# Optimization experiments

Hardware: AMD Instinct MI355X
Metric: run time of the kernel (lower is better)

Reference implementation:

```python
import jax, jax.numpy as jnp
import numpy as np
import math

D_MODEL = 1024
NUM_HEADS = 16
D_K = D_MODEL // NUM_HEADS
ROPE_THETA = 10000.0


def _rope(x, pos):
    # x: [b, h, s, d], pos: [s] int -> apply interleaved rotary embedding
    d = x.shape[-1]
    inv_freq = 1.0 / (ROPE_THETA ** (jnp.arange(0, d, 2, dtype=jnp.float32) / d))  # [d/2]
    angles = pos.astype(jnp.float32)[:, None] * inv_freq  # [s, d/2]
    cos = jnp.cos(angles)  # broadcast to [1,1,s,d/2]
    sin = jnp.sin(angles)
    x1 = x[..., 0::2]
    x2 = x[..., 1::2]
    o1 = x1 * cos - x2 * sin
    o2 = x1 * sin + x2 * cos
    return jnp.stack([o1, o2], axis=-1).reshape(x.shape)


def setup_inputs() -> dict:
    key = jax.random.key(0)
    kx, kq, kk, kv, ko = jax.random.split(key, 5)
    scale = 1.0 / math.sqrt(D_MODEL)
    x = jax.random.normal(kx, (2, 2048, D_MODEL), dtype=jnp.float32)
    token_positions = jnp.arange(2048, dtype=jnp.int32)
    Wq = jax.random.normal(kq, (D_MODEL, D_MODEL), dtype=jnp.float32) * scale
    Wk = jax.random.normal(kk, (D_MODEL, D_MODEL), dtype=jnp.float32) * scale
    Wv = jax.random.normal(kv, (D_MODEL, D_MODEL), dtype=jnp.float32) * scale
    Wo = jax.random.normal(ko, (D_MODEL, D_MODEL), dtype=jnp.float32) * scale
    return {"x": x, "token_positions": token_positions, "Wq": Wq, "Wk": Wk, "Wv": Wv, "Wo": Wo}


def reference(x, token_positions, Wq, Wk, Wv, Wo):
    b, s, _ = x.shape
    h, dk = NUM_HEADS, D_K
    # Linear stores weight as [out, in]; y = x @ W.T
    def proj(W):
        y = jnp.einsum('bsm,nm->bsn', x, W)
        return y.reshape(b, s, h, dk).transpose(0, 2, 1, 3)  # [b,h,s,dk]
    Q = _rope(proj(Wq), token_positions)
    K = _rope(proj(Wk), token_positions)
    V = proj(Wv)
    scores = jnp.einsum('bhqd,bhkd->bhqk', Q, K) / math.sqrt(dk)
    causal = jnp.arange(s)[:, None] >= jnp.arange(s)[None, :]  # [s,s]
    scores = jnp.where(causal, scores, -jnp.inf)
    weights = jax.nn.softmax(scores, axis=-1)
    attn = jnp.einsum('bhqk,bhkd->bhqd', weights, V)  # [b,h,s,dk]
    attn = attn.transpose(0, 2, 1, 3).reshape(b, s, h * dk)
    return jnp.einsum('bsn,mn->bsm', attn, Wo)
```

## Files before the change

kernel.cpp:

```cpp
#include <hip/hip_runtime.h>
#include <math.h>

#define SEQ   2048
#define BATCH 2
#define NH    16
#define DKD   64
#define DM    1024
#define MTOT  (BATCH*SEQ)

typedef short bf16x8 __attribute__((ext_vector_type(8)));
typedef float f32x4  __attribute__((ext_vector_type(4)));
typedef unsigned short u16x4 __attribute__((ext_vector_type(4)));
typedef unsigned short u16x8 __attribute__((ext_vector_type(8)));

#define MFMA_B16(a,b,c) __builtin_amdgcn_mfma_f32_16x16x32_bf16((a),(b),(c),0,0,0)

__device__ __forceinline__ unsigned short f2bf(float f) {
    union { float f; unsigned int u; } v; v.f = f;
    unsigned int r = v.u + 0x7FFFu + ((v.u >> 16) & 1u);
    return (unsigned short)(r >> 16);
}
__device__ __forceinline__ float bf2f(unsigned short h) {
    union { unsigned int u; float f; } v; v.u = ((unsigned int)h) << 16;
    return v.f;
}
__device__ __forceinline__ void gload16(const void* g, void* l) {
    __builtin_amdgcn_global_load_lds(
        (const __attribute__((address_space(1))) unsigned int*)g,
        (__attribute__((address_space(3))) unsigned int*)l, 16, 0, 0);
}

__global__ __launch_bounds__(256)
void convert_all(const float* __restrict__ x,  const float* __restrict__ Wq,
                 const float* __restrict__ Wk, const float* __restrict__ Wv,
                 const float* __restrict__ Wo,
                 unsigned short* __restrict__ Xb, unsigned short* __restrict__ Wqkvb,
                 unsigned short* __restrict__ Wob)
{
    int i = blockIdx.x * 256 + threadIdx.x;
    const float* src;
    unsigned short* dst;
    size_t off;
    if (i < (1 << 19)) {
        src = x; dst = Xb; off = (size_t)i;
    } else {
        int j = i - (1 << 19);
        int wsel = j >> 17;
        off = (size_t)(j & ((1 << 17) - 1));
        src = (wsel == 0) ? Wq : (wsel == 1) ? Wk : (wsel == 2) ? Wv : Wo;
        dst = (wsel < 3) ? Wqkvb + (size_t)wsel * (1u << 20) : Wob;
    }
    float4 v0 = ((const float4*)src)[off * 2];
    float4 v1 = ((const float4*)src)[off * 2 + 1];
    u16x8 o = { f2bf(v0.x), f2bf(v0.y), f2bf(v0.z), f2bf(v0.w),
                f2bf(v1.x), f2bf(v1.y), f2bf(v1.z), f2bf(v1.w) };
    *(u16x8*)&dst[off * 8] = o;
}

__global__ __launch_bounds__(256)
void rope_bf16(unsigned short* __restrict__ Qb, unsigned short* __restrict__ Kb,
               const int* __restrict__ pos)
{
    int idx = blockIdx.x * 256 + threadIdx.x;
    int tsel = idx >> 19;
    int i = idx & ((1 << 19) - 1);
    unsigned short* base = tsel ? Kb : Qb;
    int d8 = i & 7;
    int s  = (i >> 3) & (SEQ - 1);
    float P = (float)pos[s];
    const float NEG_L2 = -0.41524101186092103f;

    u16x8 v = *(u16x8*)&base[(size_t)i * 8];
    u16x8 o;
    #pragma unroll
    for (int k = 0; k < 4; ++k) {
        int pi = d8 * 4 + k;
        float ang = P * exp2f((float)pi * NEG_L2);
        float sn, cs;
        sincosf(ang, &sn, &cs);
        float e0 = bf2f(v[2*k]), e1 = bf2f(v[2*k + 1]);
        o[2*k]     = f2bf(e0 * cs - e1 * sn);
        o[2*k + 1] = f2bf(e0 * sn + e1 * cs);
    }
    *(u16x8*)&base[(size_t)i * 8] = o;
}

template<int MODE>
__global__ __launch_bounds__(512)
void gemm_mfma(const unsigned short* __restrict__ A, const unsigned short* __restrict__ B,
               unsigned short* __restrict__ Qb, unsigned short* __restrict__ Kb,
               unsigned short* __restrict__ VTb, float* __restrict__ Cf)
{
    const int t = threadIdx.x;
    const int w = t >> 6, l = t & 63, lid = l & 15, hi = (l >> 4) * 16;
    const int wm = w >> 2, wn = w & 3;
    const int m0 = blockIdx.y * 128, n0 = blockIdx.x * 128;

    __shared__ __align__(16) char At[3][8192];
    __shared__ __align__(16) char Bt[3][8192];

    f32x4 acc[4][2];
    const f32x4 z4 = {0.f, 0.f, 0.f, 0.f};
    #pragma unroll
    for (int i = 0; i < 4; ++i)
        #pragma unroll
        for (int j2 = 0; j2 < 2; ++j2) acc[i][j2] = z4;

    const char* Ab = (const char*)A;
    const char* Bb = (const char*)B;

    auto stage = [&](int buf, int kt) {
        const int kbyte = kt * 64;
        int o   = t * 16;
        int row = o >> 6, cb = o & 63;
        int sw  = ((row >> 1) & 3) << 4;
        gload16(Ab + (size_t)(m0 + row) * 2048 + kbyte + (cb ^ sw), At[buf] + w * 1024);
        gload16(Bb + (size_t)(n0 + row) * 2048 + kbyte + (cb ^ sw), Bt[buf] + w * 1024);
    };

    const int NKT = DM / 32;
    stage(0, 0);
    stage(1, 1);

    for (int kt = 0; kt < NKT; ++kt) {
        const int cur = kt % 3;
        if (kt == NKT - 1) asm volatile("s_waitcnt vmcnt(0)" ::: "memory");
        else               asm volatile("s_waitcnt vmcnt(2)" ::: "memory");
        __builtin_amdgcn_s_barrier();
        if (kt + 2 < NKT) stage((kt + 2) % 3, kt + 2);

        bf16x8 af[4], bfr[2];
        #pragma unroll
        for (int mf = 0; mf < 4; ++mf) {
            int ar = wm * 64 + mf * 16 + lid;
            af[mf] = *(const bf16x8*)(At[cur] + ar * 64 + (hi ^ (((ar >> 1) & 3) << 4)));
        }
        #pragma unroll
        for (int nf = 0; nf < 2; ++nf) {
            int br = wn * 32 + nf * 16 + lid;
            bfr[nf] = *(const bf16x8*)(Bt[cur] + br * 64 + (hi ^ (((br >> 1) & 3) << 4)));
        }
        __builtin_amdgcn_s_setprio(1);
        #pragma unroll
        for (int mf = 0; mf < 4; ++mf)
            #pragma unroll
            for (int nf = 0; nf < 2; ++nf)
                acc[mf][nf] = MFMA_B16(af[mf], bfr[nf], acc[mf][nf]);
        __builtin_amdgcn_s_setprio(0);
    }

    if (MODE == 1) {
        #pragma unroll
        for (int mf = 0; mf < 4; ++mf)
            #pragma unroll
            for (int nf = 0; nf < 2; ++nf) {
                int ncol = n0 + wn * 32 + nf * 16 + lid;
                #pragma unroll
                for (int jj = 0; jj < 4; ++jj) {
                    int mrow = m0 + wm * 64 + mf * 16 + (l >> 4) * 4 + jj;
                    Cf[(size_t)mrow * DM + ncol] = acc[mf][nf][jj];
                }
            }
    } else {
        const int z = n0 >> 10;
        const int nbase = n0 & 1023;
        #pragma unroll
        for (int mf = 0; mf < 4; ++mf)
            #pragma unroll
            for (int nf = 0; nf < 2; ++nf) {
                int ncol = nbase + wn * 32 + nf * 16 + lid;
                int h = ncol >> 6, d = ncol & 63;
                int mbase = m0 + wm * 64 + mf * 16 + (l >> 4) * 4;
                int b = mbase >> 11, s0v = mbase & 2047;
                if (z == 2) {
                    u16x4 pk = { f2bf(acc[mf][nf][0]), f2bf(acc[mf][nf][1]),
                                 f2bf(acc[mf][nf][2]), f2bf(acc[mf][nf][3]) };
                    *(u16x4*)&VTb[((size_t)(b * NH + h) * DKD + d) * SEQ + s0v] = pk;
                } else {
                    unsigned short* dst = (z == 0) ? Qb : Kb;
                    #pragma unroll
                    for (int jj = 0; jj < 4; ++jj)
                        dst[((size_t)(b * NH + h) * SEQ + (s0v + jj)) * DKD + d] =
                            f2bf(acc[mf][nf][jj]);
                }
            }
    }
}

__global__ __launch_bounds__(1024, 8)
void flash_mfma(const unsigned short* __restrict__ Qb, const unsigned short* __restrict__ Kb,
                const unsigned short* __restrict__ VTb, unsigned short* __restrict__ AOb)
{
    const int L  = blockIdx.y * 16 + blockIdx.x;
    const int g  = L >> 8, c = L & 255;
    const int j  = c & 15;
    const int bh = (g << 4) | (c >> 4);
    const int b = bh >> 4, h = bh & 15;
    const int qbA = g ? (30 - 2 * j) : (2 * j);
    const int qbB = qbA + 1;

    const int t = threadIdx.x;
    const int w8 = t >> 6, l = t & 63, lid = l & 15, hi = (l >> 4) * 16;
    const int h4 = l >> 4;
    const int tile = w8 >> 3, wq = (w8 >> 1) & 3, kh = w8 & 1;
    const int qbMy = tile ? qbB : qbA;
    const int ntMy = qbMy + 1;
    const int q0My = qbMy * 64;
    const int ntB  = qbB + 1;

    __shared__ __align__(16) char Kt[3][8192];
    __shared__ __align__(16) char Vt[3][8192];
    __shared__ __align__(16) char Pt[2][8192];

    const char* Kbh = (const char*)(Kb  + (size_t)bh * SEQ * DKD);
    const char* Vbh = (const char*)(VTb + (size_t)bh * SEQ * DKD);
    const char* Qbh = (const char*)(Qb  + (size_t)bh * SEQ * DKD);

    const f32x4 z4 = {0.f, 0.f, 0.f, 0.f};
    const int qrow = wq * 16 + lid;
    const float CLOG = 0.18033688011112042f;
    const float NMC  = -17.312340490667560f;

    bf16x8 onesv;
    #pragma unroll
    for (int i = 0; i < 8; ++i) onesv[i] = (short)0x3F80;

    bf16x8 qf[2];
    qf[0] = *(const bf16x8*)(Qbh + (size_t)(q0My + qrow) * 128 + 0  + hi);
    qf[1] = *(const bf16x8*)(Qbh + (size_t)(q0My + qrow) * 128 + 64 + hi);

    f32x4 o[4], o5;
    #pragma unroll
    for (int nf = 0; nf < 4; ++nf) o[nf] = z4;
    o5 = z4;

    auto stage = [&](int buf, int kt) {
        if (t < 512) {
            int o_ = t * 16, row = o_ >> 7, cl = o_ & 127, sw = (row & 7) << 4;
            gload16(Kbh + (size_t)(kt * 64 + row) * 128 + (cl ^ sw),
                    Kt[buf] + w8 * 1024);
        } else {
            int o_ = (t - 512) * 16, row = o_ >> 7, cl = o_ & 127, sw = (row & 7) << 4;
            gload16(Vbh + (size_t)row * (SEQ * 2) + kt * 128 + (cl ^ sw),
                    Vt[buf] + (w8 - 8) * 1024);
        }
    };

    stage(0, 0);
    stage(1, 1);

    for (int kt = 0; kt < ntB; ++kt) {
        const int cur = kt % 3;

        if (kt == ntB - 1) asm volatile("s_waitcnt vmcnt(0)" ::: "memory");
        else               asm volatile("s_waitcnt vmcnt(1)" ::: "memory");
        __builtin_amdgcn_s_barrier();
        if (kt + 2 < ntB) stage((kt + 2) % 3, kt + 2);

        if (kt < ntMy) {
            f32x4 sf[2];
            __builtin_amdgcn_s_setprio(1);
            #pragma unroll
            for (int nf = 0; nf < 2; ++nf) {
                f32x4 a = z4;
                #pragma unroll
                for (int ks = 0; ks < 2; ++ks) {
                    int r  = kh * 32 + nf * 16 + lid;
                    int cb = ks * 64 + hi;
                    bf16x8 kfr = *(const bf16x8*)(Kt[cur] + r * 128 + (cb ^ ((r & 7) << 4)));
                    a = MFMA_B16(kfr, qf[ks], a);
                }
                sf[nf] = a;
            }
            __builtin_amdgcn_s_setprio(0);

            if (kt == qbMy) {
                const int qloc = wq * 16 + lid;
                #pragma unroll
                for (int nf = 0; nf < 2; ++nf) {
                    #pragma unroll
                    for (int jj = 0; jj < 4; ++jj) {
                        int keyloc = kh * 32 + nf * 16 + h4 * 4 + jj;
                        if (keyloc > qloc) sf[nf][jj] = -1e30f;
                    }
                }
            }

            uint2 pk[2];
            #pragma unroll
            for (int nf = 0; nf < 2; ++nf) {
                float p0, p1, p2, p3;
                asm("v_exp_f32 %0, %1" : "=v"(p0) : "v"(fmaf(sf[nf][0], CLOG, NMC)));
                asm("v_exp_f32 %0, %1" : "=v"(p1) : "v"(fmaf(sf[nf][1], CLOG, NMC)));
                asm("v_exp_f32 %0, %1" : "=v"(p2) : "v"(fmaf(sf[nf][2], CLOG, NMC)));
                asm("v_exp_f32 %0, %1" : "=v"(p3) : "v"(fmaf(sf[nf][3], CLOG, NMC)));
                unsigned plo, phi;
                asm("v_cvt_pk_bf16_f32 %0, %1, %2" : "=v"(plo) : "v"(p0), "v"(p1));
                asm("v_cvt_pk_bf16_f32 %0, %1, %2" : "=v"(phi) : "v"(p2), "v"(p3));
                pk[nf].x = plo; pk[nf].y = phi;
            }

            {
                const int swz  = (lid & 7) << 4;
                char* base = Pt[tile] + qrow * 128;
                #pragma unroll
                for (int nf = 0; nf < 2; ++nf)
                    *(uint2*)(base + ((kh * 64 + nf * 32 + 8 * h4) ^ swz)) = pk[nf];
            }

            {
                int cb = kh * 64 + hi;
                bf16x8 pa = *(const bf16x8*)(Pt[tile] + qrow * 128 + (cb ^ ((qrow & 7) << 4)));
                __builtin_amdgcn_s_setprio(1);
                #pragma unroll
                for (int nf = 0; nf < 4; ++nf) {
                    int dr = nf * 16 + lid;
                    bf16x8 vb = *(const bf16x8*)(Vt[cur] + dr * 128 + (cb ^ ((dr & 7) << 4)));
                    o[nf] = MFMA_B16(pa, vb, o[nf]);
                }
                o5 = MFMA_B16(pa, onesv, o5);
                __builtin_amdgcn_s_setprio(0);
            }
        }
    }

    __syncthreads();
    const int ww = w8 >> 1;
    char* scr = (ww < 4) ? ((char*)Kt + ww * 5120)
                         : ((char*)Vt + (ww - 4) * 5120);
    if (kh == 1) {
        #pragma unroll
        for (int nf = 0; nf < 4; ++nf)
            *(f32x4*)(scr + l * 80 + nf * 16) = o[nf];
        *(f32x4*)(scr + l * 80 + 64) = o5;
    }
    __syncthreads();
    if (kh == 0) {
        #pragma unroll
        for (int nf = 0; nf < 4; ++nf) {
            f32x4 po = *(const f32x4*)(scr + l * 80 + nf * 16);
            o[nf] += po;
        }
        f32x4 po5 = *(const f32x4*)(scr + l * 80 + 64);
        o5 += po5;

        float inv[4];
        #pragma unroll
        for (int jj = 0; jj < 4; ++jj) inv[jj] = 1.0f / o5[jj];
        #pragma unroll
        for (int nf = 0; nf < 4; ++nf)
            #pragma unroll
            for (int jj = 0; jj < 4; ++jj) {
                int srow = q0My + wq * 16 + h4 * 4 + jj;
                int col  = h * 64 + nf * 16 + lid;
                AOb[((size_t)b * SEQ + srow) * DM + col] = f2bf(o[nf][jj] * inv[jj]);
            }
    }
}

extern "C" void kernel_launch(void* const* d_in, const int* in_sizes, int n_in,
                              void* d_out, int out_size, void* d_ws, size_t ws_size,
                              hipStream_t stream)
{
    const float* x   = (const float*)d_in[0];
    const int*   pos = (const int*)  d_in[1];
    const float* Wq  = (const float*)d_in[2];
    const float* Wk  = (const float*)d_in[3];
    const float* Wv  = (const float*)d_in[4];
    const float* Wo  = (const float*)d_in[5];
    float* out = (float*)d_out;

    const size_t M1 = 1u << 20;
    unsigned short* ws  = (unsigned short*)d_ws;
    unsigned short* Xb    = ws;
    unsigned short* Wqkvb = ws + 4 * M1;
    unsigned short* Wob   = ws + 7 * M1;
    unsigned short* Qbf   = ws + 8 * M1;
    unsigned short* Kbf   = ws + 12 * M1;
    unsigned short* VTb   = ws + 16 * M1;
    unsigned short* AOb   = ws + 20 * M1;

    convert_all<<<4096, 256, 0, stream>>>(x, Wq, Wk, Wv, Wo, Xb, Wqkvb, Wob);

    gemm_mfma<0><<<dim3(24, 32), 512, 0, stream>>>(Xb, Wqkvb, Qbf, Kbf, VTb, nullptr);

    rope_bf16<<<4096, 256, 0, stream>>>(Qbf, Kbf, pos);

    flash_mfma<<<dim3(16, 32), 1024, 0, stream>>>(Qbf, Kbf, VTb, AOb);

    gemm_mfma<1><<<dim3(8, 32), 512, 0, stream>>>(AOb, Wob, nullptr, nullptr, nullptr, out);
}
```

Measured before the change: 107.2 us.

## Double GEMM block to 1024 threads with 2x8 wave grid, split A/B loads

The projection GEMM kernel now runs 16 waves per 128x128 tile in place of 8, so each wave computes a 64x16 sub-tile with half the accumulators. Global-to-LDS staging is split so the first 512 threads load A and the rest load B, and the vmcnt wait drops to one outstanding load per thread. The aim is more waves in flight to hide latency and lower register pressure. The cost is more A-fragment LDS reads per MFMA, since each wave reloads four A fragments for a single B fragment, plus more barrier participants.

Result: faster. 101.6 us, median of 3 (-5.2%).

```diff
diff --git a/kernel.cpp b/kernel.cpp
--- a/kernel.cpp
+++ b/kernel.cpp
@@ -86,36 +86,38 @@
 }
 
 template<int MODE>
-__global__ __launch_bounds__(512)
+__global__ __launch_bounds__(1024, 8)
 void gemm_mfma(const unsigned short* __restrict__ A, const unsigned short* __restrict__ B,
                unsigned short* __restrict__ Qb, unsigned short* __restrict__ Kb,
                unsigned short* __restrict__ VTb, float* __restrict__ Cf)
 {
     const int t = threadIdx.x;
     const int w = t >> 6, l = t & 63, lid = l & 15, hi = (l >> 4) * 16;
-    const int wm = w >> 2, wn = w & 3;
+    const int wm = w >> 3, wn = w & 7;
     const int m0 = blockIdx.y * 128, n0 = blockIdx.x * 128;
 
     __shared__ __align__(16) char At[3][8192];
     __shared__ __align__(16) char Bt[3][8192];
 
-    f32x4 acc[4][2];
+    f32x4 acc[4];
     const f32x4 z4 = {0.f, 0.f, 0.f, 0.f};
     #pragma unroll
-    for (int i = 0; i < 4; ++i)
-        #pragma unroll
-        for (int j2 = 0; j2 < 2; ++j2) acc[i][j2] = z4;
+    for (int i = 0; i < 4; ++i) acc[i] = z4;
 
     const char* Ab = (const char*)A;
     const char* Bb = (const char*)B;
 
     auto stage = [&](int buf, int kt) {
         const int kbyte = kt * 64;
-        int o   = t * 16;
+        int o   = (t & 511) * 16;
         int row = o >> 6, cb = o & 63;
         int sw  = ((row >> 1) & 3) << 4;
-        gload16(Ab + (size_t)(m0 + row) * 2048 + kbyte + (cb ^ sw), At[buf] + w * 1024);
-        gload16(Bb + (size_t)(n0 + row) * 2048 + kbyte + (cb ^ sw), Bt[buf] + w * 1024);
+        if (t < 512)
+            gload16(Ab + (size_t)(m0 + row) * 2048 + kbyte + (cb ^ sw),
+                    At[buf] + w * 1024);
+        else
+            gload16(Bb + (size_t)(n0 + row) * 2048 + kbyte + (cb ^ sw),
+                    Bt[buf] + (w - 8) * 1024);
     };
 
     const int NKT = DM / 32;
@@ -125,65 +127,58 @@
     for (int kt = 0; kt < NKT; ++kt) {
         const int cur = kt % 3;
         if (kt == NKT - 1) asm volatile("s_waitcnt vmcnt(0)" ::: "memory");
-        else               asm volatile("s_waitcnt vmcnt(2)" ::: "memory");
+        else               asm volatile("s_waitcnt vmcnt(1)" ::: "memory");
         __builtin_amdgcn_s_barrier();
         if (kt + 2 < NKT) stage((kt + 2) % 3, kt + 2);
 
-        bf16x8 af[4], bfr[2];
+        bf16x8 af[4], bfr;
         #pragma unroll
         for (int mf = 0; mf < 4; ++mf) {
             int ar = wm * 64 + mf * 16 + lid;
             af[mf] = *(const bf16x8*)(At[cur] + ar * 64 + (hi ^ (((ar >> 1) & 3) << 4)));
         }
-        #pragma unroll
-        for (int nf = 0; nf < 2; ++nf) {
-            int br = wn * 32 + nf * 16 + lid;
-            bfr[nf] = *(const bf16x8*)(Bt[cur] + br * 64 + (hi ^ (((br >> 1) & 3) << 4)));
+        {
+            int br = wn * 16 + lid;
+            bfr = *(const bf16x8*)(Bt[cur] + br * 64 + (hi ^ (((br >> 1) & 3) << 4)));
         }
         __builtin_amdgcn_s_setprio(1);
         #pragma unroll
         for (int mf = 0; mf < 4; ++mf)
+            acc[mf] = MFMA_B16(af[mf], bfr, acc[mf]);
+        __builtin_amdgcn_s_setprio(0);
+    }
+
+    if (MODE == 1) {
+        #pragma unroll
+        for (int mf = 0; mf < 4; ++mf) {
+            int ncol = n0 + wn * 16 + lid;
             #pragma unroll
-            for (int nf = 0; nf < 2; ++nf)
-                acc[mf][nf] = MFMA_B16(af[mf], bfr[nf], acc[mf][nf]);
-        __builtin_amdgcn_s_setprio(0);
-    }
-
-    if (MODE == 1) {
-        #pragma unroll
-        for (int mf = 0; mf < 4; ++mf)
-            #pragma unroll
-            for (int nf = 0; nf < 2; ++nf) {
-                int ncol = n0 + wn * 32 + nf * 16 + lid;
-                #pragma unroll
-                for (int jj = 0; jj < 4; ++jj) {
-                    int mrow = m0 + wm * 64 + mf * 16 + (l >> 4) * 4 + jj;
-                    Cf[(size_t)mrow * DM + ncol] = acc[mf][nf][jj];
-                }
-            }
+            for (int jj = 0; jj < 4; ++jj) {
+                int mrow = m0 + wm * 64 + mf * 16 + (l >> 4) * 4 + jj;
+                Cf[(size_t)mrow * DM + ncol] = acc[mf][jj];
+            }
+        }
     } else {
         const int z = n0 >> 10;
         const int nbase = n0 & 1023;
         #pragma unroll
-        for (int mf = 0; mf < 4; ++mf)
-            #pragma unroll
-            for (int nf = 0; nf < 2; ++nf) {
-                int ncol = nbase + wn * 32 + nf * 16 + lid;
-                int h = ncol >> 6, d = ncol & 63;
-                int mbase = m0 + wm * 64 + mf * 16 + (l >> 4) * 4;
-                int b = mbase >> 11, s0v = mbase & 2047;
-                if (z == 2) {
-                    u16x4 pk = { f2bf(acc[mf][nf][0]), f2bf(acc[mf][nf][1]),
-                                 f2bf(acc[mf][nf][2]), f2bf(acc[mf][nf][3]) };
-                    *(u16x4*)&VTb[((size_t)(b * NH + h) * DKD + d) * SEQ + s0v] = pk;
-                } else {
-                    unsigned short* dst = (z == 0) ? Qb : Kb;
-                    #pragma unroll
-                    for (int jj = 0; jj < 4; ++jj)
-                        dst[((size_t)(b * NH + h) * SEQ + (s0v + jj)) * DKD + d] =
-                            f2bf(acc[mf][nf][jj]);
-                }
-            }
+        for (int mf = 0; mf < 4; ++mf) {
+            int ncol = nbase + wn * 16 + lid;
+            int h = ncol >> 6, d = ncol & 63;
+            int mbase = m0 + wm * 64 + mf * 16 + (l >> 4) * 4;
+            int b = mbase >> 11, s0v = mbase & 2047;
+            if (z == 2) {
+                u16x4 pk = { f2bf(acc[mf][0]), f2bf(acc[mf][1]),
+                             f2bf(acc[mf][2]), f2bf(acc[mf][3]) };
+                *(u16x4*)&VTb[((size_t)(b * NH + h) * DKD + d) * SEQ + s0v] = pk;
+            } else {
+                unsigned short* dst = (z == 0) ? Qb : Kb;
+                #pragma unroll
+                for (int jj = 0; jj < 4; ++jj)
+                    dst[((size_t)(b * NH + h) * SEQ + (s0v + jj)) * DKD + d] =
+                        f2bf(acc[mf][jj]);
+            }
+        }
     }
 }
 
@@ -382,11 +377,11 @@
 
     convert_all<<<4096, 256, 0, stream>>>(x, Wq, Wk, Wv, Wo, Xb, Wqkvb, Wob);
 
-    gemm_mfma<0><<<dim3(24, 32), 512, 0, stream>>>(Xb, Wqkvb, Qbf, Kbf, VTb, nullptr);
+    gemm_mfma<0><<<dim3(24, 32), 1024, 0, stream>>>(Xb, Wqkvb, Qbf, Kbf, VTb, nullptr);
 
     rope_bf16<<<4096, 256, 0, stream>>>(Qbf, Kbf, pos);
 
     flash_mfma<<<dim3(16, 32), 1024, 0, stream>>>(Qbf, Kbf, VTb, AOb);
 
-    gemm_mfma<1><<<dim3(8, 32), 512, 0, stream>>>(AOb, Wob, nullptr, nullptr, nullptr, out);
-}
+    gemm_mfma<1><<<dim3(8, 32), 1024, 0, stream>>>(AOb, Wob, nullptr, nullptr, nullptr, out);
+}
```
